# Kernel tuning notes

Hardware: AMD Instinct MI355X
Metric: run time of the kernel (lower is better)

The kernel has to match this reference:

```python
import jax, jax.numpy as jnp
import numpy as np

EPS = 1e-5
GROUPS = 8

def group_norm(x, gamma, beta):
    # x: [B,C,H,W], 8 groups
    B, C, H, W = x.shape
    xg = x.reshape(B, GROUPS, C // GROUPS, H, W)
    mu = jnp.mean(xg, axis=(2, 3, 4), keepdims=True)
    var = jnp.mean((xg - mu) ** 2, axis=(2, 3, 4), keepdims=True)
    xn = ((xg - mu) * jax.lax.rsqrt(var + EPS)).reshape(B, C, H, W)
    return xn * gamma[None, :, None, None] + beta[None, :, None, None]

def setup_inputs() -> dict:
    key = jax.random.key(0)
    ks = jax.random.split(key, 7)
    B, C, H, W = 4, 256, 64, 64
    x = jax.random.normal(ks[0], (B, C, H, W), dtype=jnp.float32)
    gamma = jnp.ones((C,), dtype=jnp.float32)
    beta = jnp.zeros((C,), dtype=jnp.float32)
    s = 1.0 / np.sqrt(C)
    w_qkv = jax.random.normal(ks[1], (3 * C, C), dtype=jnp.float32) * s
    b_qkv = jnp.zeros((3 * C,), dtype=jnp.float32)
    w_proj = jax.random.normal(ks[2], (C, C), dtype=jnp.float32) * s
    b_proj = jnp.zeros((C,), dtype=jnp.float32)
    return {"x": x, "gamma": gamma, "beta": beta, "w_qkv": w_qkv,
            "b_qkv": b_qkv, "w_proj": w_proj, "b_proj": b_proj}

def reference(x, gamma, beta, w_qkv, b_qkv, w_proj, b_proj):
    B, C, H, W = x.shape
    N = H * W
    h = group_norm(x, gamma, beta)
    # 1x1 conv == per-pixel matmul
    qkv = jnp.einsum('bchw,oc->bohw', h, w_qkv) + b_qkv[None, :, None, None]
    q, k, v = jnp.split(qkv, 3, axis=1)  # each [B,C,H,W]
    q = q.reshape(B, C, N).transpose(0, 2, 1)   # [B,N,C]
    k = k.reshape(B, C, N)                      # [B,C,N]
    v = v.reshape(B, C, N).transpose(0, 2, 1)   # [B,N,C]
    attn = jax.nn.softmax(jnp.einsum('bnc,bcm->bnm', q, k) / jnp.sqrt(jnp.float32(C)), axis=-1)
    out = jnp.einsum('bnm,bmc->bnc', attn, v)   # [B,N,C]
    out = out.transpose(0, 2, 1).reshape(B, C, H, W)
    proj = jnp.einsum('bchw,oc->bohw', out, w_proj) + b_proj[None, :, None, None]
    return x + proj
```

## Files before the change

### kernel.cpp

```cpp
#include <hip/hip_runtime.h>
#include <hip/hip_bf16.h>
#include <math.h>

#define B 4
#define C 256
#define G 8
#define N 4096
#define EPSV 1e-5f
#define QSCALE 0.0901684400f
#define THR2 11.5416f

typedef __attribute__((ext_vector_type(8))) short short8;
typedef __attribute__((ext_vector_type(16))) float f32x16;
typedef unsigned short ushort_t;
typedef unsigned int uint_t;

__device__ __forceinline__ ushort_t f2bf(float f) {
    union { float f; uint_t u; } c; c.f = f;
    uint_t u = c.u;
    uint_t r = (u + 0x7FFFu + ((u >> 16) & 1u)) >> 16;
    return (ushort_t)r;
}
__device__ __forceinline__ float bf2f(ushort_t h) {
    union { uint_t u; float f; } c; c.u = ((uint_t)h) << 16;
    return c.f;
}
__device__ __forceinline__ uint_t pack2(float a, float b) {
    return (uint_t)f2bf(a) | ((uint_t)f2bf(b) << 16);
}
__device__ __forceinline__ uint_t cvtpk_bf16(float lo, float hi) {
    uint_t r;
    asm("v_cvt_pk_bf16_f32 %0, %1, %2" : "=v"(r) : "v"(lo), "v"(hi));
    return r;
}
__device__ __forceinline__ float fexp2(float x) {
    return __builtin_amdgcn_exp2f(x);
}
__device__ __forceinline__ void gl_lds16(const void* g, void* l) {
    __builtin_amdgcn_global_load_lds(
        (const __attribute__((address_space(1))) void*)g,
        (__attribute__((address_space(3))) void*)l, 16, 0, 0);
}

__global__ __launch_bounds__(256) void gn_wconv(const float* __restrict__ x,
        float* __restrict__ partials, const float* __restrict__ wq,
        const float* __restrict__ wp, ushort_t* __restrict__ wbf) {
    int blk = blockIdx.x;
    if (blk < 256) {
        int bg = blk >> 3;
        int part = blk & 7;
        const float4* xp4 = (const float4*)(x + (size_t)bg * (32 * N) + (size_t)part * (32 * N / 8));
        float s = 0.f, ss = 0.f;
        for (int i = threadIdx.x; i < 4096; i += 256) {
            float4 v = xp4[i];
            s  += v.x + v.y + v.z + v.w;
            ss += v.x*v.x + v.y*v.y + v.z*v.z + v.w*v.w;
        }
        __shared__ float rs[256], rss[256];
        rs[threadIdx.x] = s; rss[threadIdx.x] = ss;
        __syncthreads();
        for (int off = 128; off > 0; off >>= 1) {
            if (threadIdx.x < off) {
                rs[threadIdx.x]  += rs[threadIdx.x + off];
                rss[threadIdx.x] += rss[threadIdx.x + off];
            }
            __syncthreads();
        }
        if (threadIdx.x == 0) {
            partials[(bg*8 + part)*2]     = rs[0];
            partials[(bg*8 + part)*2 + 1] = rss[0];
        }
    } else {
        int idx = (blk - 256)*256 + threadIdx.x;
        #pragma unroll
        for (int p = 0; p < 4; p++) {
            int id = idx + p*16384;
            float4 v = (id < 49152) ? ((const float4*)wq)[id] : ((const float4*)wp)[id - 49152];
            uint2 pk; pk.x = pack2(v.x, v.y); pk.y = pack2(v.z, v.w);
            *(uint2*)&wbf[(size_t)id*4] = pk;
        }
    }
}

__global__ __launch_bounds__(256) void qkv_fused(const float* __restrict__ x,
        const ushort_t* __restrict__ wbf, const float* __restrict__ gamma,
        const float* __restrict__ beta, const float* __restrict__ partials,
        const float* __restrict__ bias,
        ushort_t* __restrict__ qbf, ushort_t* __restrict__ kimg, ushort_t* __restrict__ vimg) {
    int b = blockIdx.z, o0 = blockIdx.y*128, n0 = blockIdx.x*128;
    int tid = threadIdx.x;
    int w = tid>>6, l = tid&63, l31 = l&31, lh = l>>5;
    int cg = tid >> 5;
    int nq = tid & 31;
    __shared__ short Ws[2][8192];
    __shared__ short Hs[2][8192];
    __shared__ float sst[16];

    if (tid < 8) {
        float s = 0.f, ss = 0.f;
        #pragma unroll
        for (int p = 0; p < 8; p++) {
            s  += partials[((b*8 + tid)*8 + p)*2];
            ss += partials[((b*8 + tid)*8 + p)*2 + 1];
        }
        const float inv = 1.f / 131072.f;
        float mu = s * inv;
        float var = fmaxf(ss * inv - mu*mu, 0.f);
        sst[tid*2]     = mu;
        sst[tid*2 + 1] = rsqrtf(var + EPSV);
    }
    __syncthreads();

    const ushort_t* wb = wbf + (size_t)o0*256;

    auto stageW = [&](int bb, int c0) {
        #pragma unroll
        for (int q = 0; q < 4; q++) {
            int u0 = (q*4 + w)*64;
            int u  = u0 + l;
            int row = u & 127, ch = u >> 7;
            gl_lds16(wb + (size_t)row*256 + c0 + ch*8, &Ws[bb][u0*8]);
        }
    };
    auto loadX = [&](int c0, float4* xv) {
        const float* xb = x + ((size_t)b*C + c0 + cg*8)*N + n0 + nq*4;
        #pragma unroll
        for (int e = 0; e < 8; e++)
            xv[e] = *(const float4*)(xb + (size_t)e*N);
    };
    auto writeH = [&](int bb, int c0, const float4* xv) {
        int cbase = c0 + cg*8;
        int g = cbase >> 5;
        float mu = sst[g*2], rs = sst[g*2+1];
        float ga[8], be[8];
        #pragma unroll
        for (int e = 0; e < 8; e++) {
            float gm = gamma[cbase+e];
            ga[e] = gm*rs;
            be[e] = beta[cbase+e] - mu*ga[e];
        }
        #pragma unroll
        for (int j = 0; j < 4; j++) {
            float h[8];
            #pragma unroll
            for (int e = 0; e < 8; e++) {
                float vx = (j==0) ? xv[e].x : (j==1) ? xv[e].y : (j==2) ? xv[e].z : xv[e].w;
                h[e] = vx*ga[e] + be[e];
            }
            uint4 pk;
            pk.x = pack2(h[0], h[1]);
            pk.y = pack2(h[2], h[3]);
            pk.z = pack2(h[4], h[5]);
            pk.w = pack2(h[6], h[7]);
            *(uint4*)&Hs[bb][(size_t)(cg*128 + nq*4 + j)*8] = pk;
        }
    };

    f32x16 acc[4];
    #pragma unroll
    for (int nf = 0; nf < 4; nf++)
        #pragma unroll
        for (int r = 0; r < 16; r++) acc[nf][r] = 0.f;

    float4 xv[8];
    loadX(0, xv);
    stageW(0, 0);
    writeH(0, 0, xv);
    __syncthreads();

    for (int t = 0; t < 4; t++) {
        int bb = t & 1;
        if (t < 3) { stageW(bb^1, (t+1)*64); loadX((t+1)*64, xv); }
        short8 af[4];
        #pragma unroll
        for (int s = 0; s < 4; s++)
            af[s] = *(const short8*)&Ws[bb][((2*s+lh)*128 + w*32 + l31)*8];
        #pragma unroll
        for (int nf = 0; nf < 4; nf++) {
            #pragma unroll
            for (int s = 0; s < 4; s++) {
                short8 hf = *(const short8*)&Hs[bb][((2*s+lh)*128 + nf*32 + l31)*8];
                acc[nf] = __builtin_amdgcn_mfma_f32_32x32x16_bf16(af[s], hf, acc[nf], 0, 0, 0);
            }
        }
        if (t < 3) writeH(bb^1, (t+1)*64, xv);
        __syncthreads();
    }

    int ow = o0 + w*32;
    float bv[16];
    #pragma unroll
    for (int r = 0; r < 16; r++) bv[r] = bias[ow + (r&3) + 8*(r>>2) + 4*lh];

    if (ow < 256) {
        #pragma unroll
        for (int nf = 0; nf < 4; nf++) {
            int n = n0 + nf*32 + l31;
            ushort_t* row = qbf + ((size_t)(b*N + n))*256 + ow;
            #pragma unroll
            for (int rp = 0; rp < 8; rp++) {
                int r0 = rp*2;
                int cl = (r0&3) + 8*(r0>>2) + 4*lh;
                uint_t wd = cvtpk_bf16((acc[nf][r0]+bv[r0])*QSCALE, (acc[nf][r0+1]+bv[r0+1])*QSCALE);
                *(uint_t*)(row + cl) = wd;
            }
        }
    } else if (ow < 512) {
        int cb = ow - 256;
        #pragma unroll
        for (int nf = 0; nf < 4; nf++) {
            int n = n0 + nf*32 + l31;
            ushort_t* tbase = kimg + (size_t)b*1048576 + (size_t)(n>>5)*8192
                            + (size_t)l31*8 + 4*lh;
            #pragma unroll
            for (int g = 0; g < 4; g++) {
                uint2 pk;
                pk.x = pack2(acc[nf][g*4+0]+bv[g*4+0], acc[nf][g*4+1]+bv[g*4+1]);
                pk.y = pack2(acc[nf][g*4+2]+bv[g*4+2], acc[nf][g*4+3]+bv[g*4+3]);
                *(uint2*)(tbase + (size_t)((cb>>3)+g)*256) = pk;
            }
        }
    } else {
        int cb = ow - 512;
        #pragma unroll
        for (int nf = 0; nf < 4; nf++) {
            int n = n0 + nf*32 + l31;
            ushort_t* tbase = vimg + (size_t)b*1048576 + (size_t)(n>>5)*8192
                            + (size_t)(l31>>3)*2048 + (l31&7);
            #pragma unroll
            for (int r = 0; r < 16; r++) {
                int cl = (r&3) + 8*(r>>2) + 4*lh;
                tbase[(size_t)(cb+cl)*8] = f2bf(acc[nf][r] + bv[r]);
            }
        }
    }
}

__global__ __launch_bounds__(256, 2) void attn_mfma(const ushort_t* __restrict__ qbf,
        const ushort_t* __restrict__ kimg, const ushort_t* __restrict__ vimg,
        ushort_t* __restrict__ part, float* __restrict__ ml) {
    int f = blockIdx.x;
    int comb = f & 15;
    int qt  = f >> 4;
    int b   = comb >> 2;
    int kvq = comb & 3;
    constexpr int NT = 32;
    int w = threadIdx.x >> 6;
    int l = threadIdx.x & 63;
    int l31 = l & 31, lh = l >> 5;

    __shared__ short KV[2][2][8192];

    int qbase = qt*128 + w*32;
    short8 qf[16];
    {
        const ushort_t* qrow = qbf + ((size_t)(b*N + qbase + l31))*256;
        #pragma unroll
        for (int s = 0; s < 16; s++)
            qf[s] = *(const short8*)(qrow + s*16 + lh*8);
    }

    f32x16 ot[8];
    #pragma unroll
    for (int mc = 0; mc < 8; mc++)
        #pragma unroll
        for (int r = 0; r < 16; r++) ot[mc][r] = 0.f;
    float m = -INFINITY, lsum = 0.f;

    const char* kbase = (const char*)kimg + (size_t)b*2097152;
    const char* vbase = (const char*)vimg + (size_t)b*2097152;

    auto stage = [&](int slot, int t) {
        int tile = kvq*32 + t;
        const char* kt = kbase + (size_t)tile*16384;
        const char* vt = vbase + (size_t)tile*16384;
        #pragma unroll
        for (int q = 0; q < 4; q++) {
            int u0 = (w*4 + q)*64;
            gl_lds16(kt + (u0 + l)*16, &KV[slot][0][u0*8]);
            gl_lds16(vt + (u0 + l)*16, &KV[slot][1][u0*8]);
        }
    };

    stage(0, 0);

    for (int t = 0; t < NT; t++) {
        int slot = t & 1;
        __syncthreads();
        if (t+1 < NT) stage(slot^1, t+1);

        f32x16 st0, st1;
        #pragma unroll
        for (int r = 0; r < 16; r++) { st0[r] = 0.f; st1[r] = 0.f; }
        const short* kb_ = &KV[slot][0][0];
        __builtin_amdgcn_s_setprio(1);
        #pragma unroll
        for (int s = 0; s < 8; s++) {
            short8 ka = *(const short8*)(kb_ + ((size_t)((4*s   + lh)*32 + l31))*8);
            short8 kc = *(const short8*)(kb_ + ((size_t)((4*s+2 + lh)*32 + l31))*8);
            st0 = __builtin_amdgcn_mfma_f32_32x32x16_bf16(ka, qf[2*s],   st0, 0, 0, 0);
            st1 = __builtin_amdgcn_mfma_f32_32x32x16_bf16(kc, qf[2*s+1], st1, 0, 0, 0);
        }
        __builtin_amdgcn_s_setprio(0);

        float sv[16];
        #pragma unroll
        for (int r = 0; r < 16; r++) sv[r] = st0[r] + st1[r];

        float a0 = fmaxf(sv[0], sv[1]),  a1 = fmaxf(sv[2], sv[3]);
        float a2 = fmaxf(sv[4], sv[5]),  a3 = fmaxf(sv[6], sv[7]);
        float a4 = fmaxf(sv[8], sv[9]),  a5 = fmaxf(sv[10], sv[11]);
        float a6 = fmaxf(sv[12], sv[13]), a7 = fmaxf(sv[14], sv[15]);
        float b0 = fmaxf(a0, a1), b1 = fmaxf(a2, a3), b2 = fmaxf(a4, a5), b3 = fmaxf(a6, a7);
        float pmax = fmaxf(fmaxf(b0, b1), fmaxf(b2, b3));
        pmax = fmaxf(pmax, __shfl_xor(pmax, 32));
        if (!__all(pmax <= m + THR2)) {
            float mn = fmaxf(m, pmax);
            float fac = fexp2(m - mn);
            m = mn;
            lsum *= fac;
            #pragma unroll
            for (int mc = 0; mc < 8; mc++)
                #pragma unroll
                for (int r = 0; r < 16; r++) ot[mc][r] *= fac;
        }
        float p[16];
        #pragma unroll
        for (int r = 0; r < 16; r++) p[r] = fexp2(sv[r] - m);
        float s0_ = (p[0]+p[1]) + (p[2]+p[3]);
        float s1_ = (p[4]+p[5]) + (p[6]+p[7]);
        float s2_ = (p[8]+p[9]) + (p[10]+p[11]);
        float s3_ = (p[12]+p[13]) + (p[14]+p[15]);
        float ls = (s0_+s1_) + (s2_+s3_);
        ls += __shfl_xor(ls, 32);
        lsum += ls;

        short8 pf0, pf1;
        {
            uint_t x0 = cvtpk_bf16(p[0], p[1]);
            uint_t y0 = cvtpk_bf16(p[4], p[5]);
            uint_t x1 = cvtpk_bf16(p[2], p[3]);
            uint_t y1 = cvtpk_bf16(p[6], p[7]);
            auto r0 = __builtin_amdgcn_permlane32_swap(x0, y0, false, false);
            auto r1 = __builtin_amdgcn_permlane32_swap(x1, y1, false, false);
            union { uint_t u[4]; short8 s8; } u_;
            u_.u[0] = r0[0]; u_.u[1] = r1[0]; u_.u[2] = r0[1]; u_.u[3] = r1[1];
            pf0 = u_.s8;
            uint_t x2 = cvtpk_bf16(p[8],  p[9]);
            uint_t y2 = cvtpk_bf16(p[12], p[13]);
            uint_t x3 = cvtpk_bf16(p[10], p[11]);
            uint_t y3 = cvtpk_bf16(p[14], p[15]);
            auto r2 = __builtin_amdgcn_permlane32_swap(x2, y2, false, false);
            auto r3 = __builtin_amdgcn_permlane32_swap(x3, y3, false, false);
            union { uint_t u[4]; short8 s8; } u2_;
            u2_.u[0] = r2[0]; u2_.u[1] = r3[0]; u2_.u[2] = r2[1]; u2_.u[3] = r3[1];
            pf1 = u2_.s8;
        }

        const short* vb_ = &KV[slot][1][0];
        __builtin_amdgcn_s_setprio(1);
        #pragma unroll
        for (int mc = 0; mc < 8; mc++) {
            short8 v0 = *(const short8*)(vb_ + ((size_t)((lh)*256   + mc*32 + l31))*8);
            short8 v1 = *(const short8*)(vb_ + ((size_t)((2+lh)*256 + mc*32 + l31))*8);
            ot[mc] = __builtin_amdgcn_mfma_f32_32x32x16_bf16(v0, pf0, ot[mc], 0, 0, 0);
            ot[mc] = __builtin_amdgcn_mfma_f32_32x32x16_bf16(v1, pf1, ot[mc], 0, 0, 0);
        }
        __builtin_amdgcn_s_setprio(0);
    }

    float invl = 1.f / lsum;
    ushort_t* pbase = part + (size_t)kvq*4194304 + ((size_t)(b*N + qbase + l31))*256;
    #pragma unroll
    for (int mc = 0; mc < 8; mc++)
        #pragma unroll
        for (int rp = 0; rp < 8; rp++) {
            int r0 = rp*2;
            uint_t wd = cvtpk_bf16(ot[mc][r0]*invl, ot[mc][r0+1]*invl);
            int c0 = (r0 & 3) + 8*(r0 >> 2) + 4*lh + 32*mc;
            *(uint_t*)(pbase + c0) = wd;
        }
    if (l < 32) {
        size_t row = (size_t)kvq*16384 + b*4096 + qbase + l;
        ml[row*2]     = m;
        ml[row*2 + 1] = lsum;
    }
}

__global__ __launch_bounds__(256) void proj_merge(const ushort_t* __restrict__ part,
        const float* __restrict__ ml, const ushort_t* __restrict__ wpbf,
        const float* __restrict__ bp, const float* __restrict__ x, float* __restrict__ out) {
    int b = blockIdx.z, o0 = blockIdx.y*128, n0 = blockIdx.x*64;
    int tid = threadIdx.x;
    int w = tid>>6, l = tid&63, l31 = l&31, lh = l>>5;
    __shared__ short Ws[2][8192];
    __shared__ short Hs[2][4096];

    const ushort_t* wb = wpbf + (size_t)o0*256;

    int srow = tid & 63;
    int ch0  = tid >> 6;
    size_t rowbase = ((size_t)(b*4096 + n0 + srow))*256;
    float wv[4];
    {
        float mv[4], lv[4];
        #pragma unroll
        for (int i = 0; i < 4; i++) {
            size_t rr = (size_t)i*16384 + b*4096 + n0 + srow;
            mv[i] = ml[rr*2];
            lv[i] = ml[rr*2 + 1];
        }
        float M = fmaxf(fmaxf(mv[0], mv[1]), fmaxf(mv[2], mv[3]));
        float wsum = 0.f;
        #pragma unroll
        for (int i = 0; i < 4; i++) { wv[i] = fexp2(mv[i] - M)*lv[i]; wsum += wv[i]; }
        float inv = 1.f / wsum;
        #pragma unroll
        for (int i = 0; i < 4; i++) wv[i] *= inv;
    }

    auto stageW = [&](int bb, int c0) {
        #pragma unroll
        for (int q = 0; q < 4; q++) {
            int u0 = (q*4 + w)*64;
            int u  = u0 + l;
            int row = u & 127, ch = u >> 7;
            gl_lds16(wb + (size_t)row*256 + c0 + ch*8, &Ws[bb][u0*8]);
        }
    };
    short8 hA[4], hB[4];
    auto Hload = [&](int c0) {
        #pragma unroll
        for (int i = 0; i < 4; i++) {
            const ushort_t* pp = part + (size_t)i*4194304 + rowbase + c0;
            hA[i] = *(const short8*)(pp + ch0*8);
            hB[i] = *(const short8*)(pp + (ch0+4)*8);
        }
    };
    auto Hwrite = [&](int bb) {
        float oA[8], oB[8];
        #pragma unroll
        for (int e = 0; e < 8; e++) { oA[e] = 0.f; oB[e] = 0.f; }
        #pragma unroll
        for (int i = 0; i < 4; i++) {
            float wi = wv[i];
            #pragma unroll
            for (int e = 0; e < 8; e++) {
                oA[e] += wi*bf2f((ushort_t)hA[i][e]);
                oB[e] += wi*bf2f((ushort_t)hB[i][e]);
            }
        }
        uint4 pkA, pkB;
        pkA.x = pack2(oA[0], oA[1]); pkA.y = pack2(oA[2], oA[3]);
        pkA.z = pack2(oA[4], oA[5]); pkA.w = pack2(oA[6], oA[7]);
        pkB.x = pack2(oB[0], oB[1]); pkB.y = pack2(oB[2], oB[3]);
        pkB.z = pack2(oB[4], oB[5]); pkB.w = pack2(oB[6], oB[7]);
        *(uint4*)&Hs[bb][(size_t)(ch0*64 + srow)*8]     = pkA;
        *(uint4*)&Hs[bb][(size_t)((ch0+4)*64 + srow)*8] = pkB;
    };

    f32x16 acc[2];
    #pragma unroll
    for (int nf = 0; nf < 2; nf++)
        #pragma unroll
        for (int r = 0; r < 16; r++) acc[nf][r] = 0.f;

    stageW(0, 0);
    Hload(0);
    Hwrite(0);
    __syncthreads();
    for (int t = 0; t < 4; t++) {
        int bb = t & 1;
        if (t < 3) { stageW(bb^1, (t+1)*64); Hload((t+1)*64); }
        short8 af[4];
        #pragma unroll
        for (int s = 0; s < 4; s++)
            af[s] = *(const short8*)&Ws[bb][((2*s+lh)*128 + w*32 + l31)*8];
        #pragma unroll
        for (int nf = 0; nf < 2; nf++) {
            #pragma unroll
            for (int s = 0; s < 4; s++) {
                short8 hf = *(const short8*)&Hs[bb][((2*s+lh)*64 + nf*32 + l31)*8];
                acc[nf] = __builtin_amdgcn_mfma_f32_32x32x16_bf16(af[s], hf, acc[nf], 0, 0, 0);
            }
        }
        if (t < 3) Hwrite(bb^1);
        __syncthreads();
    }

    int cw = o0 + w*32;
    float bv[16];
    #pragma unroll
    for (int r = 0; r < 16; r++) bv[r] = bp[cw + (r&3) + 8*(r>>2) + 4*lh];

    #pragma unroll
    for (int nf = 0; nf < 2; nf++) {
        int n = n0 + nf*32 + l31;
        #pragma unroll
        for (int r = 0; r < 16; r++) {
            int cl = (r&3) + 8*(r>>2) + 4*lh;
            size_t a = ((size_t)b*C + cw + cl)*N + n;
            out[a] = acc[nf][r] + bv[r] + x[a];
        }
    }
}

extern "C" void kernel_launch(void* const* d_in, const int* in_sizes, int n_in,
                              void* d_out, int out_size, void* d_ws, size_t ws_size,
                              hipStream_t stream) {
    const float* x      = (const float*)d_in[0];
    const float* gamma  = (const float*)d_in[1];
    const float* beta   = (const float*)d_in[2];
    const float* w_qkv  = (const float*)d_in[3];
    const float* b_qkv  = (const float*)d_in[4];
    const float* w_proj = (const float*)d_in[5];
    const float* b_proj = (const float*)d_in[6];
    float* out = (float*)d_out;
    char* wsb  = (char*)d_ws;

    const size_t MB = 1048576;
    ushort_t* qbf  = (ushort_t*)(wsb);
    ushort_t* kimg = (ushort_t*)(wsb + 8*MB);
    ushort_t* vimg = (ushort_t*)(wsb + 16*MB);
    ushort_t* part = (ushort_t*)(wsb + 24*MB);
    float*    ml   = (float*)  (wsb + 56*MB);
    float* partials = (float*) (wsb + 56*MB + 524288);
    ushort_t* wbf  = (ushort_t*)(wsb + 56*MB + 528384);

    gn_wconv<<<dim3(320), dim3(256), 0, stream>>>(x, partials, w_qkv, w_proj, wbf);
    qkv_fused<<<dim3(32, 6, 4), dim3(256), 0, stream>>>(x, wbf, gamma, beta, partials, b_qkv, qbf, kimg, vimg);
    attn_mfma<<<dim3(512), dim3(256), 0, stream>>>(qbf, kimg, vimg, part, ml);
    proj_merge<<<dim3(64, 2, 4), dim3(256), 0, stream>>>(part, ml, wbf + 196608, b_proj, x, out);
}
```

Measured before the change: 137.9 us.

## Software-pipeline QK^T of next tile with softmax and PV of current tile

The attention loop now issues the QK^T MFMAs for tile t+1 before running the softmax and PV MFMAs for tile t, and alternates two score accumulators across a 2-way unrolled loop. K stays double-buffered, V moves to a triple buffer, and global-to-LDS prefetch runs two tiles ahead. The aim is to hide exp, reduction and conversion latency behind matrix-core work and to give loads more time to land. The cost is more LDS per block (80 KB instead of 64 KB, which could limit occupancy) and more register pressure. The QK^T chain also becomes one serial accumulator instead of two interleaved ones.

```diff
diff --git a/kernel.cpp b/kernel.cpp
--- a/kernel.cpp
+++ b/kernel.cpp
@@ -249,7 +249,8 @@
     int l = threadIdx.x & 63;
     int l31 = l & 31, lh = l >> 5;
 
-    __shared__ short KV[2][2][8192];
+    __shared__ short Kl[2][8192];
+    __shared__ short Vl[3][8192];
 
     int qbase = qt*128 + w*32;
     short8 qf[16];
@@ -270,47 +271,42 @@
     const char* kbase = (const char*)kimg + (size_t)b*2097152;
     const char* vbase = (const char*)vimg + (size_t)b*2097152;
 
-    auto stage = [&](int slot, int t) {
-        int tile = kvq*32 + t;
+    auto stage = [&](int j) {
+        int tile = kvq*32 + j;
         const char* kt = kbase + (size_t)tile*16384;
         const char* vt = vbase + (size_t)tile*16384;
+        short* kd = &Kl[j & 1][0];
+        short* vd = &Vl[j % 3][0];
         #pragma unroll
         for (int q = 0; q < 4; q++) {
             int u0 = (w*4 + q)*64;
-            gl_lds16(kt + (u0 + l)*16, &KV[slot][0][u0*8]);
-            gl_lds16(vt + (u0 + l)*16, &KV[slot][1][u0*8]);
-        }
-    };
-
-    stage(0, 0);
-
-    for (int t = 0; t < NT; t++) {
-        int slot = t & 1;
+            gl_lds16(kt + (u0 + l)*16, kd + u0*8);
+            gl_lds16(vt + (u0 + l)*16, vd + u0*8);
+        }
+    };
+
+    auto qk_issue = [&](int j, f32x16& s) {
+        #pragma unroll
+        for (int r = 0; r < 16; r++) s[r] = 0.f;
+        const short* kb_ = &Kl[j & 1][0];
+        __builtin_amdgcn_s_setprio(1);
+        #pragma unroll
+        for (int s2 = 0; s2 < 16; s2++) {
+            short8 ka = *(const short8*)(kb_ + ((size_t)((2*s2 + lh)*32 + l31))*8);
+            s = __builtin_amdgcn_mfma_f32_32x32x16_bf16(ka, qf[s2], s, 0, 0, 0);
+        }
+        __builtin_amdgcn_s_setprio(0);
+    };
+
+    auto body = [&](int t, f32x16& cur, f32x16& nxt) {
         __syncthreads();
-        if (t+1 < NT) stage(slot^1, t+1);
-
-        f32x16 st0, st1;
-        #pragma unroll
-        for (int r = 0; r < 16; r++) { st0[r] = 0.f; st1[r] = 0.f; }
-        const short* kb_ = &KV[slot][0][0];
-        __builtin_amdgcn_s_setprio(1);
-        #pragma unroll
-        for (int s = 0; s < 8; s++) {
-            short8 ka = *(const short8*)(kb_ + ((size_t)((4*s   + lh)*32 + l31))*8);
-            short8 kc = *(const short8*)(kb_ + ((size_t)((4*s+2 + lh)*32 + l31))*8);
-            st0 = __builtin_amdgcn_mfma_f32_32x32x16_bf16(ka, qf[2*s],   st0, 0, 0, 0);
-            st1 = __builtin_amdgcn_mfma_f32_32x32x16_bf16(kc, qf[2*s+1], st1, 0, 0, 0);
-        }
-        __builtin_amdgcn_s_setprio(0);
-
-        float sv[16];
-        #pragma unroll
-        for (int r = 0; r < 16; r++) sv[r] = st0[r] + st1[r];
-
-        float a0 = fmaxf(sv[0], sv[1]),  a1 = fmaxf(sv[2], sv[3]);
-        float a2 = fmaxf(sv[4], sv[5]),  a3 = fmaxf(sv[6], sv[7]);
-        float a4 = fmaxf(sv[8], sv[9]),  a5 = fmaxf(sv[10], sv[11]);
-        float a6 = fmaxf(sv[12], sv[13]), a7 = fmaxf(sv[14], sv[15]);
+        if (t+1 < NT) qk_issue(t+1, nxt);
+        if (t+2 < NT) stage(t+2);
+
+        float a0 = fmaxf(cur[0], cur[1]),  a1 = fmaxf(cur[2], cur[3]);
+        float a2 = fmaxf(cur[4], cur[5]),  a3 = fmaxf(cur[6], cur[7]);
+        float a4 = fmaxf(cur[8], cur[9]),  a5 = fmaxf(cur[10], cur[11]);
+        float a6 = fmaxf(cur[12], cur[13]), a7 = fmaxf(cur[14], cur[15]);
         float b0 = fmaxf(a0, a1), b1 = fmaxf(a2, a3), b2 = fmaxf(a4, a5), b3 = fmaxf(a6, a7);
         float pmax = fmaxf(fmaxf(b0, b1), fmaxf(b2, b3));
         pmax = fmaxf(pmax, __shfl_xor(pmax, 32));
@@ -324,32 +320,31 @@
                 #pragma unroll
                 for (int r = 0; r < 16; r++) ot[mc][r] *= fac;
         }
-        float p[16];
-        #pragma unroll
-        for (int r = 0; r < 16; r++) p[r] = fexp2(sv[r] - m);
-        float s0_ = (p[0]+p[1]) + (p[2]+p[3]);
-        float s1_ = (p[4]+p[5]) + (p[6]+p[7]);
-        float s2_ = (p[8]+p[9]) + (p[10]+p[11]);
-        float s3_ = (p[12]+p[13]) + (p[14]+p[15]);
+        #pragma unroll
+        for (int r = 0; r < 16; r++) cur[r] = fexp2(cur[r] - m);
+        float s0_ = (cur[0]+cur[1]) + (cur[2]+cur[3]);
+        float s1_ = (cur[4]+cur[5]) + (cur[6]+cur[7]);
+        float s2_ = (cur[8]+cur[9]) + (cur[10]+cur[11]);
+        float s3_ = (cur[12]+cur[13]) + (cur[14]+cur[15]);
         float ls = (s0_+s1_) + (s2_+s3_);
         ls += __shfl_xor(ls, 32);
         lsum += ls;
 
         short8 pf0, pf1;
         {
-            uint_t x0 = cvtpk_bf16(p[0], p[1]);
-            uint_t y0 = cvtpk_bf16(p[4], p[5]);
-            uint_t x1 = cvtpk_bf16(p[2], p[3]);
-            uint_t y1 = cvtpk_bf16(p[6], p[7]);
+            uint_t x0 = cvtpk_bf16(cur[0], cur[1]);
+            uint_t y0 = cvtpk_bf16(cur[4], cur[5]);
+            uint_t x1 = cvtpk_bf16(cur[2], cur[3]);
+            uint_t y1 = cvtpk_bf16(cur[6], cur[7]);
             auto r0 = __builtin_amdgcn_permlane32_swap(x0, y0, false, false);
             auto r1 = __builtin_amdgcn_permlane32_swap(x1, y1, false, false);
             union { uint_t u[4]; short8 s8; } u_;
             u_.u[0] = r0[0]; u_.u[1] = r1[0]; u_.u[2] = r0[1]; u_.u[3] = r1[1];
             pf0 = u_.s8;
-            uint_t x2 = cvtpk_bf16(p[8],  p[9]);
-            uint_t y2 = cvtpk_bf16(p[12], p[13]);
-            uint_t x3 = cvtpk_bf16(p[10], p[11]);
-            uint_t y3 = cvtpk_bf16(p[14], p[15]);
+            uint_t x2 = cvtpk_bf16(cur[8],  cur[9]);
+            uint_t y2 = cvtpk_bf16(cur[12], cur[13]);
+            uint_t x3 = cvtpk_bf16(cur[10], cur[11]);
+            uint_t y3 = cvtpk_bf16(cur[14], cur[15]);
             auto r2 = __builtin_amdgcn_permlane32_swap(x2, y2, false, false);
             auto r3 = __builtin_amdgcn_permlane32_swap(x3, y3, false, false);
             union { uint_t u[4]; short8 s8; } u2_;
@@ -357,7 +352,7 @@
             pf1 = u2_.s8;
         }
 
-        const short* vb_ = &KV[slot][1][0];
+        const short* vb_ = &Vl[t % 3][0];
         __builtin_amdgcn_s_setprio(1);
         #pragma unroll
         for (int mc = 0; mc < 8; mc++) {
@@ -367,6 +362,18 @@
             ot[mc] = __builtin_amdgcn_mfma_f32_32x32x16_bf16(v1, pf1, ot[mc], 0, 0, 0);
         }
         __builtin_amdgcn_s_setprio(0);
+    };
+
+    f32x16 stA, stB;
+
+    stage(0);
+    __syncthreads();
+    qk_issue(0, stA);
+    stage(1);
+
+    for (int t = 0; t < NT; t += 2) {
+        body(t,   stA, stB);
+        body(t+1, stB, stA);
     }
 
     float invl = 1.f / lsum;
```

Result: slower. 170.2 us (+23.4%).
